# Performance work log

Hardware: AMD Instinct MI355X
Metric: run time of the kernel (lower is better)

Reference implementation:

```python
import jax, jax.numpy as jnp
from jax import lax
import numpy as np

BS = 256       # batch_size
S = 16         # neighbor_samples
HOPS = 2       # context_hops
NREL = 256     # n_relations
HID = 64       # hidden dim
NENT = 100000  # n_entities
NEDGE = 1000000
PS = 8         # path_samples
PLEN = 4       # max_path_len
NPATH = 100000
RD = NREL      # feature_type='id' -> relation_dim == n_relations


def _glorot(k, shape):
    fan_in, fan_out = shape[0], shape[1]
    lim = (6.0 / (fan_in + fan_out)) ** 0.5
    return jax.random.uniform(k, shape, jnp.float32, -lim, lim)


def setup_inputs():
    key = jax.random.key(0)
    ks = jax.random.split(key, 20)
    # relation features: eye(n_relations) + zero padding row (feature_type='id')
    relation_features = jnp.concatenate(
        [jnp.eye(NREL, dtype=jnp.float32), jnp.zeros((1, NREL), jnp.float32)], axis=0)
    inp = {
        'relation_features': relation_features,
        'agg0_w': _glorot(ks[0], (RD, HID)),
        'agg0_b': jnp.zeros((HID,), jnp.float32),
        'agg1_w': _glorot(ks[1], (HID, NREL)),
        'agg1_b': jnp.zeros((NREL,), jnp.float32),
        'lstm_Wih': _glorot(ks[2], (RD, 4 * HID)),
        'lstm_Whh': _glorot(ks[3], (HID, 4 * HID)),
        'lstm_bih': jnp.zeros((4 * HID,), jnp.float32),
        'lstm_bhh': jnp.zeros((4 * HID,), jnp.float32),
        'path_w': _glorot(ks[4], (HID, NREL)),
        'path_b': jnp.zeros((NREL,), jnp.float32),
        'entity_pairs': jax.random.randint(ks[5], (BS, 2), 0, NENT),
        'train_edges': jax.random.randint(ks[6], (BS,), 0, NEDGE),
        'labels': jax.random.randint(ks[7], (BS,), 0, NREL),
        'path_ids': jax.random.randint(ks[8], (BS, PS), 0, NPATH),
        'entity2edges': jax.random.randint(ks[9], (NENT, S), 0, NEDGE),
        'edge2entities': jax.random.randint(ks[10], (NEDGE, 2), 0, NENT),
        'edge2relation': jax.random.randint(ks[11], (NEDGE,), 0, NREL),
        'id2path': jax.random.randint(ks[12], (NPATH, PLEN), 0, NREL + 1),  # NREL = padding id
        'id2length': jax.random.randint(ks[13], (NPATH,), 0, PLEN + 1),
    }
    return inp


def _lstm(x, Wih, Whh, bih, bhh):
    # x: [N, T, D] -> hs: [N, T, H]; torch gate order i, f, g, o
    N = x.shape[0]
    H = Whh.shape[0]
    b = bih + bhh

    def step(carry, xt):
        h, c = carry
        gates = xt @ Wih + h @ Whh + b
        i, f, g, o = jnp.split(gates, 4, axis=-1)
        c = jax.nn.sigmoid(f) * c + jax.nn.sigmoid(i) * jnp.tanh(g)
        h = jax.nn.sigmoid(o) * jnp.tanh(c)
        return (h, c), h

    h0 = jnp.zeros((N, H), x.dtype)
    (_, _), hs = lax.scan(step, (h0, h0), jnp.swapaxes(x, 0, 1))
    return jnp.swapaxes(hs, 0, 1)


def _forward(relation_features, agg0_w, agg0_b, agg1_w, agg1_b,
             lstm_Wih, lstm_Whh, lstm_bih, lstm_bhh, path_w, path_b,
             entity_pairs, train_edges, labels, path_ids,
             entity2edges, edge2entities, edge2relation, id2path, id2length):
    dt = relation_features.dtype
    # ---- _get_neighbors_and_masks ----
    edges_list = [labels]
    masks = []
    te = train_edges[:, None]
    neighbor_entities = entity_pairs
    for i in range(HOPS):
        if i > 0:
            neighbor_entities = edge2entities[edges_list[-1].reshape(-1)].reshape(BS, -1)
        neighbor_edges = entity2edges[neighbor_entities.reshape(-1)].reshape(BS, -1)
        edges_list.append(neighbor_edges)
        masks.append((neighbor_edges != te).astype(dt))
    # ---- gather relation features per hop ----
    edge_vectors = [relation_features[edges_list[0]]]  # [BS, RD]
    for edges in edges_list[1:]:
        rels = edge2relation[edges.reshape(-1)].reshape(edges.shape)
        edge_vectors.append(relation_features[rels])  # [BS, m, RD]
    # ---- iterative mean aggregation ----
    aggs = [(agg0_w, agg0_b, True, jax.nn.relu),
            (agg1_w, agg1_b, False, lambda x: x)]
    for i in range(HOPS):
        w, b, self_inc, act = aggs[i]
        nxt = []
        for hop in range(HOPS - i):
            d = edge_vectors[hop + 1].shape[-1]
            nv = edge_vectors[hop + 1].reshape(BS, -1, 2, S, d)
            mk = masks[hop].reshape(BS, -1, 2, S, 1)
            ev = jnp.mean(nv * mk, axis=-2)   # [BS, m, 2, d]
            out = jnp.mean(ev, axis=-2)       # [BS, m, d]
            if self_inc:
                out = out + edge_vectors[hop].reshape(BS, -1, d)
            nxt.append(act(out @ w + b))
        edge_vectors = nxt
    context_scores = edge_vectors[0].reshape(BS, NREL)
    # ---- path RNN ----
    pids = path_ids.reshape(-1)              # [BS*PS]
    paths = id2path[pids]                    # [BS*PS, PLEN]
    pf = relation_features[paths]            # [BS*PS, PLEN, RD]
    lengths = id2length[pids]                # [BS*PS]
    hs = _lstm(pf, lstm_Wih, lstm_Whh, lstm_bih, lstm_bhh)   # [BS*PS, PLEN, HID]
    padded = jnp.concatenate([jnp.zeros((hs.shape[0], 1, HID), hs.dtype), hs], axis=1)
    last = padded[jnp.arange(hs.shape[0]), lengths]          # [BS*PS, HID]
    p = (last @ path_w + path_b).reshape(BS, PS, NREL)
    path_scores = jnp.mean(p, axis=1)        # path_agg='mean'
    return jax.nn.sigmoid(context_scores + path_scores)


def reference(relation_features, agg0_w, agg0_b, agg1_w, agg1_b,
              lstm_Wih, lstm_Whh, lstm_bih, lstm_bhh, path_w, path_b,
              entity_pairs, train_edges, labels, path_ids,
              entity2edges, edge2entities, edge2relation, id2path, id2length):
    return _forward(relation_features, agg0_w, agg0_b, agg1_w, agg1_b,
                    lstm_Wih, lstm_Whh, lstm_bih, lstm_bhh, path_w, path_b,
                    entity_pairs, train_edges, labels, path_ids,
                    entity2edges, edge2entities, edge2relation, id2path, id2length)
```

## Files before the change

### kernel.cpp

```cpp
#include <hip/hip_runtime.h>
#include <math.h>

#define BS   256
#define S    16
#define NREL 256
#define HID  64
#define PS   8
#define PLEN 4
#define PPB  2
#define HOPB  1024
#define LSTMB (2048/PPB)

__device__ __forceinline__ float sigm(float x){ return 1.0f/(1.0f+expf(-x)); }
__device__ __forceinline__ float lanebc(float v, int l){
  return __uint_as_float(__builtin_amdgcn_readlane(__float_as_uint(v), l));
}

__global__ void __launch_bounds__(256) k_fused(
    const float* __restrict__ agg0_w,
    const float* __restrict__ agg0_b,
    const float* __restrict__ Wih,
    const float* __restrict__ Whh,
    const float* __restrict__ bih, const float* __restrict__ bhh,
    const int* __restrict__ entity_pairs,
    const int* __restrict__ train_edges,
    const int* __restrict__ entity2edges,
    const int* __restrict__ edge2entities,
    const int* __restrict__ edge2relation,
    const int* __restrict__ path_ids, const int* __restrict__ id2path,
    const int* __restrict__ id2length,
    float* __restrict__ ev1m, float* __restrict__ lastws){
  __shared__ float s_sc[8][32];
  __shared__ int   s_r2[8][32];
  __shared__ int   s_rel1[8];
  __shared__ float s_m0[8];
  __shared__ float s_g[4][HID];
  int blk = blockIdx.x;
  int tid = threadIdx.x, w = tid >> 6, lane = tid & 63;

  if (blk < HOPB){
    int b = blk >> 2, q = blk & 3;
    int jl = tid >> 5, slot = tid & 31;
    int j  = q*8 + jl;
    int te   = train_edges[b];
    int ent0 = entity_pairs[b*2 + (j >> 4)];
    int e1   = entity2edges[ent0*S + (j & 15)];
    int ent  = edge2entities[e1*2 + (slot >> 4)];
    int e2   = entity2edges[ent*S + (slot & 15)];
    int r2   = edge2relation[e2];
    s_r2[jl][slot] = r2;
    s_sc[jl][slot] = (e2 != te) ? (1.0f/32.0f) : 0.0f;
    if (slot == 0){
      s_rel1[jl] = edge2relation[e1];
      s_m0[jl]   = (e1 != te) ? (1.0f/32.0f) : 0.0f;
    }
    __syncthreads();
    #pragma unroll
    for (int rep = 0; rep < 2; ++rep){
      int jj = w + rep*4;
      float acc = agg0_w[s_rel1[jj]*HID + lane];
      #pragma unroll
      for (int t = 0; t < 32; ++t)
        acc += s_sc[jj][t] * agg0_w[s_r2[jj][t]*HID + lane];
      acc += agg0_b[lane];
      ev1m[(size_t)(b*32 + q*8 + jj)*HID + lane] = s_m0[jj] * fmaxf(acc, 0.f);
    }
  } else {
    int lb = blk - HOPB;
    int c = w*HID + lane;
    float wreg[HID];
    #pragma unroll
    for (int k = 0; k < HID; ++k) wreg[k] = Whh[k*256 + c];
    float bg = bih[c] + bhh[c];
    for (int p = 0; p < PPB; ++p){
      int n   = lb*PPB + p;
      int pid = path_ids[n];
      int pt0 = id2path[pid*PLEN+0];
      int pt1 = id2path[pid*PLEN+1];
      int pt2 = id2path[pid*PLEN+2];
      int pt3 = id2path[pid*PLEN+3];
      int len = id2length[pid];
      float h = 0.f, cst = 0.f;
      float h1=0.f, h2=0.f, h3=0.f, h4=0.f;
      #pragma unroll
      for (int t = 0; t < PLEN; ++t){
        int pt = (t==0)?pt0:(t==1)?pt1:(t==2)?pt2:pt3;
        float x = (pt < NREL) ? Wih[pt*256 + c] : 0.f;
        float a0=0.f, a1=0.f, a2=0.f, a3=0.f;
        #pragma unroll
        for (int k = 0; k < HID; k += 4){
          a0 += lanebc(h, k  ) * wreg[k  ];
          a1 += lanebc(h, k+1) * wreg[k+1];
          a2 += lanebc(h, k+2) * wreg[k+2];
          a3 += lanebc(h, k+3) * wreg[k+3];
        }
        s_g[w][lane] = ((a0+a1)+(a2+a3)) + x + bg;
        __syncthreads();
        float gi = s_g[0][lane], gf = s_g[1][lane],
              gg = s_g[2][lane], go = s_g[3][lane];
        __syncthreads();
        cst = sigm(gf)*cst + sigm(gi)*tanhf(gg);
        h   = sigm(go)*tanhf(cst);
        if      (t==0) h1=h;
        else if (t==1) h2=h;
        else if (t==2) h3=h;
        else           h4=h;
      }
      float last = 0.f;
      if (len >= 1) last = h1;
      if (len >= 2) last = h2;
      if (len >= 3) last = h3;
      if (len >= 4) last = h4;
      if (w == 0) lastws[(size_t)n*HID + lane] = last;
    }
  }
}

__global__ void __launch_bounds__(64) k_final(
    const float* __restrict__ ev1m,
    const float* __restrict__ lastws,
    const float* __restrict__ agg1_w,
    const float* __restrict__ agg1_b,
    const float* __restrict__ path_w,
    const float* __restrict__ path_b,
    float* __restrict__ out){
  int blk = blockIdx.x, l = threadIdx.x;
  int b = blk >> 2, q = blk & 3;
  float cs = 0.f;
  const float* src = ev1m + (size_t)b*32*HID;
  #pragma unroll 8
  for (int j = 0; j < 32; ++j) cs += src[j*HID + l];
  float als = 0.f;
  const float* sl = lastws + (size_t)b*PS*HID;
  #pragma unroll
  for (int ps = 0; ps < PS; ++ps) als += sl[ps*HID + l];
  als *= 0.125f;
  int rel = q*64 + l;
  float acc = agg1_b[rel] + path_b[rel];
  #pragma unroll 8
  for (int k = 0; k < HID; ++k)
    acc += lanebc(cs, k)*agg1_w[k*NREL + rel]
         + lanebc(als, k)*path_w[k*NREL + rel];
  out[b*NREL + rel] = 1.0f/(1.0f+expf(-acc));
}

extern "C" void kernel_launch(void* const* d_in, const int* in_sizes, int n_in,
                              void* d_out, int out_size, void* d_ws, size_t ws_size,
                              hipStream_t stream){
  const float* agg0_w   = (const float*)d_in[1];
  const float* agg0_b   = (const float*)d_in[2];
  const float* agg1_w   = (const float*)d_in[3];
  const float* agg1_b   = (const float*)d_in[4];
  const float* Wih      = (const float*)d_in[5];
  const float* Whh      = (const float*)d_in[6];
  const float* bih      = (const float*)d_in[7];
  const float* bhh      = (const float*)d_in[8];
  const float* path_w   = (const float*)d_in[9];
  const float* path_b   = (const float*)d_in[10];
  const int* entity_pairs  = (const int*)d_in[11];
  const int* train_edges   = (const int*)d_in[12];
  const int* path_ids      = (const int*)d_in[14];
  const int* entity2edges  = (const int*)d_in[15];
  const int* edge2entities = (const int*)d_in[16];
  const int* edge2relation = (const int*)d_in[17];
  const int* id2path       = (const int*)d_in[18];
  const int* id2length     = (const int*)d_in[19];

  float* ws     = (float*)d_ws;
  float* ev1m   = ws;
  float* lastws = ev1m + 524288;

  k_fused<<<HOPB + LSTMB, 256, 0, stream>>>(
      agg0_w, agg0_b, Wih, Whh, bih, bhh,
      entity_pairs, train_edges, entity2edges, edge2entities, edge2relation,
      path_ids, id2path, id2length, ev1m, lastws);
  k_final<<<BS*4, 64, 0, stream>>>(ev1m, lastws, agg1_w, agg1_b,
                                   path_w, path_b, (float*)d_out);
}
```

Baseline: 130.2 us.

## Fuse hop aggregation, LSTM, and final projection into one per-batch kernel

Replaces the two-kernel pipeline with a single kernel launched as one 512-thread block per batch element. Each block computes the hop aggregation into shared memory, runs the path LSTM in two groups of four waves, and applies the final linear layer and sigmoid directly. This removes the second launch and the global workspace round trip for intermediates. In exchange the grid shrinks from 2048 blocks to 256, each LSTM group processes its four paths sequentially, and the whole-block barriers inside the LSTM now synchronise all 8 waves, which may reduce parallelism and occupancy.

New measurement: 130.7 us. Within noise of the previous version (+0.4%).

```diff
diff --git a/kernel.cpp b/kernel.cpp
--- a/kernel.cpp
+++ b/kernel.cpp
@@ -7,21 +7,22 @@
 #define HID  64
 #define PS   8
 #define PLEN 4
-#define PPB  2
-#define HOPB  1024
-#define LSTMB (2048/PPB)
 
 __device__ __forceinline__ float sigm(float x){ return 1.0f/(1.0f+expf(-x)); }
 __device__ __forceinline__ float lanebc(float v, int l){
   return __uint_as_float(__builtin_amdgcn_readlane(__float_as_uint(v), l));
 }
 
-__global__ void __launch_bounds__(256) k_fused(
+__global__ void __launch_bounds__(512) k_all(
     const float* __restrict__ agg0_w,
     const float* __restrict__ agg0_b,
+    const float* __restrict__ agg1_w,
+    const float* __restrict__ agg1_b,
     const float* __restrict__ Wih,
     const float* __restrict__ Whh,
     const float* __restrict__ bih, const float* __restrict__ bhh,
+    const float* __restrict__ path_w,
+    const float* __restrict__ path_b,
     const int* __restrict__ entity_pairs,
     const int* __restrict__ train_edges,
     const int* __restrict__ entity2edges,
@@ -29,119 +30,127 @@
     const int* __restrict__ edge2relation,
     const int* __restrict__ path_ids, const int* __restrict__ id2path,
     const int* __restrict__ id2length,
-    float* __restrict__ ev1m, float* __restrict__ lastws){
-  __shared__ float s_sc[8][32];
-  __shared__ int   s_r2[8][32];
-  __shared__ int   s_rel1[8];
-  __shared__ float s_m0[8];
-  __shared__ float s_g[4][HID];
-  int blk = blockIdx.x;
-  int tid = threadIdx.x, w = tid >> 6, lane = tid & 63;
+    float* __restrict__ out){
+  __shared__ float s_sc[32][32];
+  __shared__ int   s_r2[32][32];
+  __shared__ int   s_rel1[32];
+  __shared__ float s_m0[32];
+  __shared__ float s_ev[32][HID];
+  __shared__ float s_last[PS][HID];
+  __shared__ float s_g[2][4][HID];
+  __shared__ float s_c[HID];
+  __shared__ float s_al[HID];
 
-  if (blk < HOPB){
-    int b = blk >> 2, q = blk & 3;
-    int jl = tid >> 5, slot = tid & 31;
-    int j  = q*8 + jl;
-    int te   = train_edges[b];
-    int ent0 = entity_pairs[b*2 + (j >> 4)];
-    int e1   = entity2edges[ent0*S + (j & 15)];
-    int ent  = edge2entities[e1*2 + (slot >> 4)];
-    int e2   = entity2edges[ent*S + (slot & 15)];
-    int r2   = edge2relation[e2];
-    s_r2[jl][slot] = r2;
-    s_sc[jl][slot] = (e2 != te) ? (1.0f/32.0f) : 0.0f;
-    if (slot == 0){
-      s_rel1[jl] = edge2relation[e1];
-      s_m0[jl]   = (e1 != te) ? (1.0f/32.0f) : 0.0f;
+  const int b   = blockIdx.x;
+  const int tid = threadIdx.x;
+  const int w   = tid >> 6, lane = tid & 63;
+  const int grp = w >> 2, gw = w & 3;
+  const int c   = gw*HID + lane;
+
+  float wreg[HID];
+  #pragma unroll
+  for (int k = 0; k < HID; ++k) wreg[k] = Whh[k*256 + c];
+  const float bg = bih[c] + bhh[c];
+
+  const int te = train_edges[b];
+
+  {
+    const int t0 = tid, t1 = tid + 512;
+    const int j0 = t0 >> 5, sl0 = t0 & 31;
+    const int j1 = t1 >> 5, sl1 = t1 & 31;
+    int ep0 = entity_pairs[b*2 + (j0 >> 4)];
+    int ep1 = entity_pairs[b*2 + (j1 >> 4)];
+    int e10 = entity2edges[ep0*S + (j0 & 15)];
+    int e11 = entity2edges[ep1*S + (j1 & 15)];
+    int en0 = edge2entities[e10*2 + (sl0 >> 4)];
+    int en1 = edge2entities[e11*2 + (sl1 >> 4)];
+    int e20 = entity2edges[en0*S + (sl0 & 15)];
+    int e21 = entity2edges[en1*S + (sl1 & 15)];
+    s_r2[j0][sl0] = edge2relation[e20];
+    s_r2[j1][sl1] = edge2relation[e21];
+    s_sc[j0][sl0] = (e20 != te) ? (1.0f/32.0f) : 0.0f;
+    s_sc[j1][sl1] = (e21 != te) ? (1.0f/32.0f) : 0.0f;
+    if (sl0 == 0){ s_rel1[j0] = edge2relation[e10];
+                   s_m0[j0]   = (e10 != te) ? (1.0f/32.0f) : 0.0f; }
+    if (sl1 == 0){ s_rel1[j1] = edge2relation[e11];
+                   s_m0[j1]   = (e11 != te) ? (1.0f/32.0f) : 0.0f; }
+  }
+  __syncthreads();
+
+  #pragma unroll
+  for (int rep = 0; rep < 4; ++rep){
+    const int j = w*4 + rep;
+    float acc = agg0_w[s_rel1[j]*HID + lane];
+    #pragma unroll
+    for (int t = 0; t < 32; ++t)
+      acc += s_sc[j][t] * agg0_w[s_r2[j][t]*HID + lane];
+    acc += agg0_b[lane];
+    s_ev[j][lane] = s_m0[j] * fmaxf(acc, 0.f);
+  }
+
+  for (int p = 0; p < 4; ++p){
+    const int n   = b*PS + grp*4 + p;
+    const int pid = path_ids[n];
+    const int pt0 = id2path[pid*PLEN+0];
+    const int pt1 = id2path[pid*PLEN+1];
+    const int pt2 = id2path[pid*PLEN+2];
+    const int pt3 = id2path[pid*PLEN+3];
+    const int len = id2length[pid];
+    float h = 0.f, cst = 0.f;
+    float h1=0.f, h2=0.f, h3=0.f, h4=0.f;
+    #pragma unroll
+    for (int t = 0; t < PLEN; ++t){
+      const int pt = (t==0)?pt0:(t==1)?pt1:(t==2)?pt2:pt3;
+      const float x = (pt < NREL) ? Wih[pt*256 + c] : 0.f;
+      float a0=0.f, a1=0.f, a2=0.f, a3=0.f;
+      #pragma unroll
+      for (int k = 0; k < HID; k += 4){
+        a0 += lanebc(h, k  ) * wreg[k  ];
+        a1 += lanebc(h, k+1) * wreg[k+1];
+        a2 += lanebc(h, k+2) * wreg[k+2];
+        a3 += lanebc(h, k+3) * wreg[k+3];
+      }
+      s_g[grp][gw][lane] = ((a0+a1)+(a2+a3)) + x + bg;
+      __syncthreads();
+      const float gi = s_g[grp][0][lane], gf = s_g[grp][1][lane],
+                  gg = s_g[grp][2][lane], go = s_g[grp][3][lane];
+      __syncthreads();
+      cst = sigm(gf)*cst + sigm(gi)*tanhf(gg);
+      h   = sigm(go)*tanhf(cst);
+      if      (t==0) h1=h;
+      else if (t==1) h2=h;
+      else if (t==2) h3=h;
+      else           h4=h;
     }
-    __syncthreads();
+    float last = 0.f;
+    if (len >= 1) last = h1;
+    if (len >= 2) last = h2;
+    if (len >= 3) last = h3;
+    if (len >= 4) last = h4;
+    if (gw == 0) s_last[grp*4 + p][lane] = last;
+  }
+  __syncthreads();
+
+  if (w == 0){
+    float cs = 0.f;
+    #pragma unroll 8
+    for (int j = 0; j < 32; ++j) cs += s_ev[j][lane];
+    s_c[lane] = cs;
+  } else if (w == 1){
+    float als = 0.f;
     #pragma unroll
-    for (int rep = 0; rep < 2; ++rep){
-      int jj = w + rep*4;
-      float acc = agg0_w[s_rel1[jj]*HID + lane];
-      #pragma unroll
-      for (int t = 0; t < 32; ++t)
-        acc += s_sc[jj][t] * agg0_w[s_r2[jj][t]*HID + lane];
-      acc += agg0_b[lane];
-      ev1m[(size_t)(b*32 + q*8 + jj)*HID + lane] = s_m0[jj] * fmaxf(acc, 0.f);
-    }
-  } else {
-    int lb = blk - HOPB;
-    int c = w*HID + lane;
-    float wreg[HID];
-    #pragma unroll
-    for (int k = 0; k < HID; ++k) wreg[k] = Whh[k*256 + c];
-    float bg = bih[c] + bhh[c];
-    for (int p = 0; p < PPB; ++p){
-      int n   = lb*PPB + p;
-      int pid = path_ids[n];
-      int pt0 = id2path[pid*PLEN+0];
-      int pt1 = id2path[pid*PLEN+1];
-      int pt2 = id2path[pid*PLEN+2];
-      int pt3 = id2path[pid*PLEN+3];
-      int len = id2length[pid];
-      float h = 0.f, cst = 0.f;
-      float h1=0.f, h2=0.f, h3=0.f, h4=0.f;
-      #pragma unroll
-      for (int t = 0; t < PLEN; ++t){
-        int pt = (t==0)?pt0:(t==1)?pt1:(t==2)?pt2:pt3;
-        float x = (pt < NREL) ? Wih[pt*256 + c] : 0.f;
-        float a0=0.f, a1=0.f, a2=0.f, a3=0.f;
-        #pragma unroll
-        for (int k = 0; k < HID; k += 4){
-          a0 += lanebc(h, k  ) * wreg[k  ];
-          a1 += lanebc(h, k+1) * wreg[k+1];
-          a2 += lanebc(h, k+2) * wreg[k+2];
-          a3 += lanebc(h, k+3) * wreg[k+3];
-        }
-        s_g[w][lane] = ((a0+a1)+(a2+a3)) + x + bg;
-        __syncthreads();
-        float gi = s_g[0][lane], gf = s_g[1][lane],
-              gg = s_g[2][lane], go = s_g[3][lane];
-        __syncthreads();
-        cst = sigm(gf)*cst + sigm(gi)*tanhf(gg);
-        h   = sigm(go)*tanhf(cst);
-        if      (t==0) h1=h;
-        else if (t==1) h2=h;
-        else if (t==2) h3=h;
-        else           h4=h;
-      }
-      float last = 0.f;
-      if (len >= 1) last = h1;
-      if (len >= 2) last = h2;
-      if (len >= 3) last = h3;
-      if (len >= 4) last = h4;
-      if (w == 0) lastws[(size_t)n*HID + lane] = last;
-    }
+    for (int ps = 0; ps < PS; ++ps) als += s_last[ps][lane];
+    s_al[lane] = als * 0.125f;
   }
-}
-
-__global__ void __launch_bounds__(64) k_final(
-    const float* __restrict__ ev1m,
-    const float* __restrict__ lastws,
-    const float* __restrict__ agg1_w,
-    const float* __restrict__ agg1_b,
-    const float* __restrict__ path_w,
-    const float* __restrict__ path_b,
-    float* __restrict__ out){
-  int blk = blockIdx.x, l = threadIdx.x;
-  int b = blk >> 2, q = blk & 3;
-  float cs = 0.f;
-  const float* src = ev1m + (size_t)b*32*HID;
-  #pragma unroll 8
-  for (int j = 0; j < 32; ++j) cs += src[j*HID + l];
-  float als = 0.f;
-  const float* sl = lastws + (size_t)b*PS*HID;
-  #pragma unroll
-  for (int ps = 0; ps < PS; ++ps) als += sl[ps*HID + l];
-  als *= 0.125f;
-  int rel = q*64 + l;
-  float acc = agg1_b[rel] + path_b[rel];
-  #pragma unroll 8
-  for (int k = 0; k < HID; ++k)
-    acc += lanebc(cs, k)*agg1_w[k*NREL + rel]
-         + lanebc(als, k)*path_w[k*NREL + rel];
-  out[b*NREL + rel] = 1.0f/(1.0f+expf(-acc));
+  __syncthreads();
+  if (tid < NREL){
+    const int rel = tid;
+    float acc = agg1_b[rel] + path_b[rel];
+    #pragma unroll 8
+    for (int k = 0; k < HID; ++k)
+      acc += s_c[k]*agg1_w[k*NREL + rel] + s_al[k]*path_w[k*NREL + rel];
+    out[b*NREL + rel] = 1.0f/(1.0f+expf(-acc));
+  }
 }
 
 extern "C" void kernel_launch(void* const* d_in, const int* in_sizes, int n_in,
@@ -166,14 +175,8 @@
   const int* id2path       = (const int*)d_in[18];
   const int* id2length     = (const int*)d_in[19];
 
-  float* ws     = (float*)d_ws;
-  float* ev1m   = ws;
-  float* lastws = ev1m + 524288;
-
-  k_fused<<<HOPB + LSTMB, 256, 0, stream>>>(
-      agg0_w, agg0_b, Wih, Whh, bih, bhh,
+  k_all<<<BS, 512, 0, stream>>>(
+      agg0_w, agg0_b, agg1_w, agg1_b, Wih, Whh, bih, bhh, path_w, path_b,
       entity_pairs, train_edges, entity2edges, edge2entities, edge2relation,
-      path_ids, id2path, id2length, ev1m, lastws);
-  k_final<<<BS*4, 64, 0, stream>>>(ev1m, lastws, agg1_w, agg1_b,
-                                   path_w, path_b, (float*)d_out);
+      path_ids, id2path, id2length, (float*)d_out);
 }
```
